# Kernel optimization log

Hardware: AMD Instinct MI355X
Metric: run time of the kernel (lower is better)

Reference implementation:

```python
import jax, jax.numpy as jnp
import numpy as np

F8 = jnp.float8_e4m3fn
FP8_MAX = 448.0  # max representable magnitude of e4m3fn


def setup_inputs() -> dict:
    key = jax.random.key(0)
    kx, kw, kb = jax.random.split(key, 3)
    x = jax.random.normal(kx, (4, 4096, 2048), dtype=jnp.float32)
    w = jax.random.normal(kw, (8192, 2048), dtype=jnp.float32) * 0.02
    bias = (jax.random.normal(kb, (8192,), dtype=jnp.float32) * 0.01).astype(jnp.float16)
    return {"x": x, "w": w, "bias": bias}


def _quantize_per_tensor(t):
    """Dynamic per-tensor symmetric fp8 quantization (mirrors the torch code).
    Returns (t_fp8, inv_scale) with inv_scale = amax / 448."""
    amax = jnp.max(jnp.abs(t))
    scale = (FP8_MAX / jnp.maximum(amax, 1e-12)).astype(jnp.float32)
    scale = jax.lax.stop_gradient(scale)  # torch computes scales under no_grad
    t_fp8 = (t * scale).astype(F8)
    return t_fp8, (1.0 / scale)


def reference(x, w, bias):
    in_features = w.shape[1]
    out_features = w.shape[0]
    x2d = x.reshape(-1, in_features)            # [M, K]
    x_fp8, inv_sx = _quantize_per_tensor(x2d)   # activation: dynamic per-tensor
    w_fp8, inv_sw = _quantize_per_tensor(w)     # weight: pre-quantized buffer + scale_w
    # _scaled_mm: fp8 GEMM accumulated in fp32, output scaled by scale_a*scale_b, cast to fp16
    acc = jnp.matmul(x_fp8.astype(jnp.float32), w_fp8.astype(jnp.float32).T)  # [M, N]
    out = (acc * (inv_sx * inv_sw)).astype(jnp.float16)
    out = out + bias  # fp16 bias epilogue
    return out.reshape(*x.shape[:-1], out_features)
```

## Files before the change

kernel.cpp:

```cpp
#include <hip/hip_runtime.h>
#include <hip/hip_fp16.h>
#include <stdint.h>
#include <stddef.h>

typedef float f32x4 __attribute__((ext_vector_type(4)));
typedef int   i32x8 __attribute__((ext_vector_type(8)));

#define GLOBAL_AS __attribute__((address_space(1)))
#define LDS_AS    __attribute__((address_space(3)))

__device__ __forceinline__ void gload_lds16(const void* g, void* l) {
    __builtin_amdgcn_global_load_lds((const GLOBAL_AS void*)g,
                                     (LDS_AS void*)l, 16, 0, 0);
}

__global__ void amax_kernel(const float* __restrict__ p, size_t n4,
                            float* __restrict__ out) {
    const float4* p4 = (const float4*)p;
    float m = 0.f;
    for (size_t i = (size_t)blockIdx.x * blockDim.x + threadIdx.x; i < n4;
         i += (size_t)gridDim.x * blockDim.x) {
        float4 v = p4[i];
        m = fmaxf(m, fmaxf(fmaxf(fabsf(v.x), fabsf(v.y)),
                           fmaxf(fabsf(v.z), fabsf(v.w))));
    }
    #pragma unroll
    for (int off = 32; off > 0; off >>= 1)
        m = fmaxf(m, __shfl_down(m, off, 64));
    __shared__ float sm[4];
    int wid = threadIdx.x >> 6;
    if ((threadIdx.x & 63) == 0) sm[wid] = m;
    __syncthreads();
    if (threadIdx.x == 0) {
        m = fmaxf(fmaxf(sm[0], sm[1]), fmaxf(sm[2], sm[3]));
        atomicMax((unsigned int*)out, __float_as_uint(m));
    }
}

__global__ void quant_kernel(const float* __restrict__ p, size_t n16,
                             const float* __restrict__ amax_p,
                             uint32_t* __restrict__ q) {
    const float scale = 448.f / fmaxf(*amax_p, 1e-12f);
    size_t i = (size_t)blockIdx.x * blockDim.x + threadIdx.x;
    if (i >= n16) return;
    const float4* src = (const float4*)p + i * 4;
    uint32_t r[4];
    #pragma unroll
    for (int j = 0; j < 4; ++j) {
        float4 v = src[j];
        uint32_t u = __builtin_amdgcn_cvt_pk_fp8_f32(v.x * scale, v.y * scale, 0u, false);
        u = __builtin_amdgcn_cvt_pk_fp8_f32(v.z * scale, v.w * scale, u, true);
        r[j] = u;
    }
    uint4 out;
    out.x = r[0]; out.y = r[1]; out.z = r[2]; out.w = r[3];
    *(uint4*)(q + i * 4) = out;
}

#define BM 128
#define BN 128
#define BK 128

__global__ __launch_bounds__(256) void gemm_mxfp8_kernel(
    const uint8_t* __restrict__ Aq,
    const uint8_t* __restrict__ Bq,
    const float* __restrict__ scal,
    const float* __restrict__ bias,
    float* __restrict__ C,
    int M, int N, int K)
{
    __shared__ __align__(16) uint8_t As[BM * BK];
    __shared__ __align__(16) uint8_t Bs[BN * BK];

    const int tid  = threadIdx.x;
    const int wid  = tid >> 6;
    const int lane = tid & 63;
    const int wm = wid >> 1, wn = wid & 1;
    const int bn = blockIdx.x, bm = blockIdx.y;
    const int r16 = lane & 15, hi = lane >> 4;

    const int srow  = wid * 8 + (lane >> 3);
    const int schunk = ((lane & 7) ^ (lane >> 3)) << 4;
    const uint8_t* Abase = Aq + (size_t)(bm * BM + srow) * K + schunk;
    const uint8_t* Bbase = Bq + (size_t)(bn * BN + srow) * K + schunk;

    const int swz = r16 & 7;
    const int u0 = ((hi * 2)     ^ swz) << 4;
    const int u1 = ((hi * 2 + 1) ^ swz) << 4;

    f32x4 acc[4][4] = {};

    for (int k0 = 0; k0 < K; k0 += BK) {
        #pragma unroll
        for (int rho = 0; rho < 4; ++rho) {
            gload_lds16(Abase + (size_t)rho * 32 * K + k0,
                        As + rho * 4096 + wid * 1024);
            gload_lds16(Bbase + (size_t)rho * 32 * K + k0,
                        Bs + rho * 4096 + wid * 1024);
        }
        __syncthreads();

        i32x8 a[4], b[4];
        #pragma unroll
        for (int mi = 0; mi < 4; ++mi) {
            const uint8_t* pa = As + (wm * 64 + mi * 16 + r16) * BK;
            int4 qa0 = *(const int4*)(pa + u0);
            int4 qa1 = *(const int4*)(pa + u1);
            a[mi] = (i32x8){qa0.x, qa0.y, qa0.z, qa0.w,
                            qa1.x, qa1.y, qa1.z, qa1.w};
            const uint8_t* pb = Bs + (wn * 64 + mi * 16 + r16) * BK;
            int4 qb0 = *(const int4*)(pb + u0);
            int4 qb1 = *(const int4*)(pb + u1);
            b[mi] = (i32x8){qb0.x, qb0.y, qb0.z, qb0.w,
                            qb1.x, qb1.y, qb1.z, qb1.w};
        }

        #pragma unroll
        for (int mi = 0; mi < 4; ++mi)
            #pragma unroll
            for (int nj = 0; nj < 4; ++nj)
                acc[mi][nj] = __builtin_amdgcn_mfma_scale_f32_16x16x128_f8f6f4(
                    a[mi], b[nj], acc[mi][nj],
                    0 , 0 ,
                    0, 0x7F7F7F7F,
                    0, 0x7F7F7F7F);
        __syncthreads();
    }

    const float sx = 448.f / fmaxf(scal[0], 1e-12f);
    const float sw = 448.f / fmaxf(scal[1], 1e-12f);
    const float inv = (1.f / sx) * (1.f / sw);

    #pragma unroll
    for (int mi = 0; mi < 4; ++mi) {
        #pragma unroll
        for (int nj = 0; nj < 4; ++nj) {
            int col = bn * BN + wn * 64 + nj * 16 + r16;
            __half hb = __float2half(bias[col]);
            #pragma unroll
            for (int r = 0; r < 4; ++r) {
                int row = bm * BM + wm * 64 + mi * 16 + hi * 4 + r;
                float v = acc[mi][nj][r] * inv;
                __half h = __hadd(__float2half(v), hb);
                C[(size_t)row * N + col] = __half2float(h);
            }
        }
    }
}

extern "C" void kernel_launch(void* const* d_in, const int* in_sizes, int n_in,
                              void* d_out, int out_size, void* d_ws, size_t ws_size,
                              hipStream_t stream) {
    const float* x    = (const float*)d_in[0];
    const float* w    = (const float*)d_in[1];
    const float* bias = (const float*)d_in[2];
    float* out = (float*)d_out;

    const int N = in_sizes[2];
    const int K = in_sizes[1] / N;
    const int M = in_sizes[0] / K;

    uint8_t* ws = (uint8_t*)d_ws;
    float* scal = (float*)ws;
    uint8_t* Aq = ws + 256;
    uint8_t* Bq = Aq + (size_t)M * K;

    hipMemsetAsync(scal, 0, 8, stream);

    amax_kernel<<<2048, 256, 0, stream>>>(x, (size_t)M * K / 4, scal);
    amax_kernel<<<2048, 256, 0, stream>>>(w, (size_t)N * K / 4, scal + 1);

    size_t nx16 = (size_t)M * K / 16;
    size_t nw16 = (size_t)N * K / 16;
    quant_kernel<<<(int)((nx16 + 255) / 256), 256, 0, stream>>>(x, nx16, scal, (uint32_t*)Aq);
    quant_kernel<<<(int)((nw16 + 255) / 256), 256, 0, stream>>>(w, nw16, scal + 1, (uint32_t*)Bq);

    dim3 grid(N / BN, M / BM);
    gemm_mxfp8_kernel<<<grid, 256, 0, stream>>>(Aq, Bq, scal, bias, out, M, N, K);
}
```

Measured before the change: 468.5 us.

## Use 256x256 tiles with 8-phase double-buffered pipelined fp8 GEMM and fused prep kernels

Replaces the 128x128 single-buffered GEMM with a 256x256 tile, 512-thread kernel that double-buffers LDS and interleaves global-to-LDS loads with MFMA phases, using explicit barriers, waitcnts and raised wave priority. It adds an XCD-aware block remap so neighbouring tiles share L2. The two amax launches and the two quantize launches are each merged into one, cutting launch overhead. The hand-tuned vmcnt scheduling assumes the load order exactly and needs K to be a multiple of 256. The 256x256 tile also means fewer blocks for the same problem.

```diff
diff --git a/kernel.cpp b/kernel.cpp
--- a/kernel.cpp
+++ b/kernel.cpp
@@ -14,12 +14,16 @@
                                      (LDS_AS void*)l, 16, 0, 0);
 }
 
-__global__ void amax_kernel(const float* __restrict__ p, size_t n4,
-                            float* __restrict__ out) {
-    const float4* p4 = (const float4*)p;
+__global__ void amax2_kernel(const float* __restrict__ x, size_t nx4,
+                             const float* __restrict__ w, size_t nw4,
+                             float* __restrict__ scal, int xblocks, int wblocks) {
+    int b = blockIdx.x;
+    const float4* p4; size_t n4; float* out; int nb; int bb;
+    if (b < xblocks) { p4 = (const float4*)x; n4 = nx4; out = scal;     nb = xblocks; bb = b; }
+    else             { p4 = (const float4*)w; n4 = nw4; out = scal + 1; nb = wblocks; bb = b - xblocks; }
     float m = 0.f;
-    for (size_t i = (size_t)blockIdx.x * blockDim.x + threadIdx.x; i < n4;
-         i += (size_t)gridDim.x * blockDim.x) {
+    for (size_t i = (size_t)bb * blockDim.x + threadIdx.x; i < n4;
+         i += (size_t)nb * blockDim.x) {
         float4 v = p4[i];
         m = fmaxf(m, fmaxf(fmaxf(fabsf(v.x), fabsf(v.y)),
                            fmaxf(fabsf(v.z), fabsf(v.w))));
@@ -37,31 +41,34 @@
     }
 }
 
-__global__ void quant_kernel(const float* __restrict__ p, size_t n16,
-                             const float* __restrict__ amax_p,
-                             uint32_t* __restrict__ q) {
-    const float scale = 448.f / fmaxf(*amax_p, 1e-12f);
-    size_t i = (size_t)blockIdx.x * blockDim.x + threadIdx.x;
-    if (i >= n16) return;
-    const float4* src = (const float4*)p + i * 4;
+__global__ void quant2_kernel(const float* __restrict__ x, const float* __restrict__ w,
+                              const float* __restrict__ scal,
+                              uint32_t* __restrict__ qx, uint32_t* __restrict__ qw,
+                              int xblocks) {
+    int b = blockIdx.x;
+    const float* src; uint32_t* dst; float sc; size_t i;
+    if (b < xblocks) { src = x; dst = qx; sc = 448.f / fmaxf(scal[0], 1e-12f);
+                       i = (size_t)b * blockDim.x + threadIdx.x; }
+    else             { src = w; dst = qw; sc = 448.f / fmaxf(scal[1], 1e-12f);
+                       i = (size_t)(b - xblocks) * blockDim.x + threadIdx.x; }
+    const float4* s4 = (const float4*)src + i * 4;
     uint32_t r[4];
     #pragma unroll
     for (int j = 0; j < 4; ++j) {
-        float4 v = src[j];
-        uint32_t u = __builtin_amdgcn_cvt_pk_fp8_f32(v.x * scale, v.y * scale, 0u, false);
-        u = __builtin_amdgcn_cvt_pk_fp8_f32(v.z * scale, v.w * scale, u, true);
+        float4 v = s4[j];
+        uint32_t u = __builtin_amdgcn_cvt_pk_fp8_f32(v.x * sc, v.y * sc, 0u, false);
+        u = __builtin_amdgcn_cvt_pk_fp8_f32(v.z * sc, v.w * sc, u, true);
         r[j] = u;
     }
-    uint4 out;
-    out.x = r[0]; out.y = r[1]; out.z = r[2]; out.w = r[3];
-    *(uint4*)(q + i * 4) = out;
-}
-
-#define BM 128
-#define BN 128
-#define BK 128
-
-__global__ __launch_bounds__(256) void gemm_mxfp8_kernel(
+    uint4 out; out.x = r[0]; out.y = r[1]; out.z = r[2]; out.w = r[3];
+    *(uint4*)(dst + i * 4) = out;
+}
+
+#define BM 256
+#define BN 256
+#define BKB 128
+
+__global__ __launch_bounds__(512, 2) void gemm_mxfp8_8p(
     const uint8_t* __restrict__ Aq,
     const uint8_t* __restrict__ Bq,
     const float* __restrict__ scal,
@@ -69,77 +76,135 @@
     float* __restrict__ C,
     int M, int N, int K)
 {
-    __shared__ __align__(16) uint8_t As[BM * BK];
-    __shared__ __align__(16) uint8_t Bs[BN * BK];
+    __shared__ __align__(16) uint8_t lds[2][2][2][128 * 128];
 
     const int tid  = threadIdx.x;
     const int wid  = tid >> 6;
     const int lane = tid & 63;
-    const int wm = wid >> 1, wn = wid & 1;
-    const int bn = blockIdx.x, bm = blockIdx.y;
+    const int wm = wid >> 2;
+    const int wn = wid & 3;
     const int r16 = lane & 15, hi = lane >> 4;
 
-    const int srow  = wid * 8 + (lane >> 3);
-    const int schunk = ((lane & 7) ^ (lane >> 3)) << 4;
-    const uint8_t* Abase = Aq + (size_t)(bm * BM + srow) * K + schunk;
-    const uint8_t* Bbase = Bq + (size_t)(bn * BN + srow) * K + schunk;
+    const int nwg = gridDim.x;
+    const int cpx = nwg >> 3;
+    const int sbid = (blockIdx.x & 7) * cpx + (blockIdx.x >> 3);
+    const int nbn = N / BN;
+    const int bn = sbid & (nbn - 1);
+    const int bm = sbid / nbn;
+
+    const uint8_t* Abase = Aq + (size_t)bm * BM * K;
+    const uint8_t* Bbase = Bq + (size_t)bn * BN * K;
+
+    const int srow = tid >> 3;
+    const int schunk16 = ((tid & 7) ^ (srow & 7)) << 4;
 
     const int swz = r16 & 7;
     const int u0 = ((hi * 2)     ^ swz) << 4;
     const int u1 = ((hi * 2 + 1) ^ swz) << 4;
 
-    f32x4 acc[4][4] = {};
-
-    for (int k0 = 0; k0 < K; k0 += BK) {
-        #pragma unroll
-        for (int rho = 0; rho < 4; ++rho) {
-            gload_lds16(Abase + (size_t)rho * 32 * K + k0,
-                        As + rho * 4096 + wid * 1024);
-            gload_lds16(Bbase + (size_t)rho * 32 * K + k0,
-                        Bs + rho * 4096 + wid * 1024);
-        }
-        __syncthreads();
-
-        i32x8 a[4], b[4];
-        #pragma unroll
-        for (int mi = 0; mi < 4; ++mi) {
-            const uint8_t* pa = As + (wm * 64 + mi * 16 + r16) * BK;
-            int4 qa0 = *(const int4*)(pa + u0);
-            int4 qa1 = *(const int4*)(pa + u1);
-            a[mi] = (i32x8){qa0.x, qa0.y, qa0.z, qa0.w,
-                            qa1.x, qa1.y, qa1.z, qa1.w};
-            const uint8_t* pb = Bs + (wn * 64 + mi * 16 + r16) * BK;
-            int4 qb0 = *(const int4*)(pb + u0);
-            int4 qb1 = *(const int4*)(pb + u1);
-            b[mi] = (i32x8){qb0.x, qb0.y, qb0.z, qb0.w,
-                            qb1.x, qb1.y, qb1.z, qb1.w};
-        }
-
-        #pragma unroll
-        for (int mi = 0; mi < 4; ++mi)
-            #pragma unroll
-            for (int nj = 0; nj < 4; ++nj)
-                acc[mi][nj] = __builtin_amdgcn_mfma_scale_f32_16x16x128_f8f6f4(
-                    a[mi], b[nj], acc[mi][nj],
-                    0 , 0 ,
-                    0, 0x7F7F7F7F,
-                    0, 0x7F7F7F7F);
-        __syncthreads();
-    }
+#define STAGE(opbase, opi, bufi, h, s)                                            \
+  { const uint8_t* g_ = (opbase) + (size_t)((h) * 128 + srow) * K + (s) * BKB + schunk16; \
+    uint8_t* l_ = &lds[bufi][opi][h][tid * 16];                                   \
+    gload_lds16(g_, l_);                                                          \
+    gload_lds16(g_ + (size_t)64 * K, l_ + 8192); }
+
+#define LDA(bufc, g)                                                              \
+  { const uint8_t* base_ = &lds[bufc][0][wm][0];                                  \
+    _Pragma("unroll") for (int j_ = 0; j_ < 4; ++j_) {                            \
+      const uint8_t* p_ = base_ + ((g) * 64 + j_ * 16 + r16) * 128;               \
+      int4 q0_ = *(const int4*)(p_ + u0);                                         \
+      int4 q1_ = *(const int4*)(p_ + u1);                                         \
+      a[j_] = (i32x8){q0_.x, q0_.y, q0_.z, q0_.w, q1_.x, q1_.y, q1_.z, q1_.w}; } }
+
+#define LDB(bufc, g)                                                              \
+  { const uint8_t* base_ = &lds[bufc][1][wn >> 1][0];                             \
+    _Pragma("unroll") for (int j_ = 0; j_ < 2; ++j_) {                            \
+      const uint8_t* p_ = base_ + ((wn & 1) * 64 + ((g) * 2 + j_) * 16 + r16) * 128; \
+      int4 q0_ = *(const int4*)(p_ + u0);                                         \
+      int4 q1_ = *(const int4*)(p_ + u1);                                         \
+      b[(g) * 2 + j_] = (i32x8){q0_.x, q0_.y, q0_.z, q0_.w, q1_.x, q1_.y, q1_.z, q1_.w}; } }
+
+#define MMA(g_m, g_n)                                                             \
+  __builtin_amdgcn_s_setprio(1);                                                  \
+  _Pragma("unroll") for (int mi_ = 0; mi_ < 4; ++mi_)                             \
+    _Pragma("unroll") for (int nj_ = 0; nj_ < 2; ++nj_)                           \
+      acc[(g_m) * 4 + mi_][(g_n) * 2 + nj_] =                                     \
+        __builtin_amdgcn_mfma_scale_f32_16x16x128_f8f6f4(                         \
+          a[mi_], b[(g_n) * 2 + nj_], acc[(g_m) * 4 + mi_][(g_n) * 2 + nj_],      \
+          0, 0, 0, 0x7F7F7F7F, 0, 0x7F7F7F7F);                                    \
+  __builtin_amdgcn_s_setprio(0);
+
+#define PH_BEGIN() do { asm volatile("" ::: "memory");                            \
+    __builtin_amdgcn_s_barrier();                                                 \
+    asm volatile("s_waitcnt lgkmcnt(0)" ::: "memory");                            \
+    __builtin_amdgcn_sched_barrier(0); } while (0)
+
+#define PH_END() do { asm volatile("" ::: "memory");                              \
+    __builtin_amdgcn_s_barrier();                                                 \
+    asm volatile("" ::: "memory"); } while (0)
+
+#define PH_END_VM(n) do { asm volatile("s_waitcnt vmcnt(" #n ")" ::: "memory");   \
+    __builtin_amdgcn_s_barrier();                                                 \
+    asm volatile("" ::: "memory"); } while (0)
+
+    f32x4 acc[8][4] = {};
+    i32x8 a[4], b[4];
+
+    STAGE(Abase, 0, 0, 0, 0);
+    STAGE(Abase, 0, 0, 1, 0);
+    STAGE(Bbase, 1, 0, 0, 0);
+    STAGE(Bbase, 1, 0, 1, 0);
+    STAGE(Bbase, 1, 1, 0, 1);
+    STAGE(Abase, 0, 1, 0, 1);
+    asm volatile("s_waitcnt vmcnt(4)" ::: "memory");
+    __builtin_amdgcn_s_barrier();
+
+#define ITER(t, LAST) do {                                                        \
+                                                    \
+    LDA(0, 0); LDB(0, 0); STAGE(Bbase, 1, 1, 1, (t) + 1);                         \
+    PH_BEGIN(); MMA(0, 0); PH_END();                                              \
+                                                           \
+    LDB(0, 1); STAGE(Abase, 0, 1, 1, (t) + 1);                                    \
+    PH_BEGIN(); MMA(0, 1); PH_END();                                              \
+                                                           \
+    LDA(0, 1); if (!(LAST)) STAGE(Bbase, 1, 0, 0, (t) + 2);                       \
+    PH_BEGIN(); MMA(1, 1); PH_END();                                              \
+                                                           \
+    if (!(LAST)) STAGE(Abase, 0, 0, 0, (t) + 2);                                  \
+    PH_BEGIN(); MMA(1, 0);                                                        \
+    if (LAST) { PH_END_VM(0); } else { PH_END_VM(4); }                            \
+                                                  \
+    LDA(1, 0); LDB(1, 0); if (!(LAST)) STAGE(Bbase, 1, 0, 1, (t) + 2);            \
+    PH_BEGIN(); MMA(0, 0); PH_END();                                              \
+                                                                          \
+    LDB(1, 1); if (!(LAST)) STAGE(Abase, 0, 0, 1, (t) + 2);                       \
+    PH_BEGIN(); MMA(0, 1); PH_END();                                              \
+                                                                          \
+    LDA(1, 1); if (!(LAST)) STAGE(Bbase, 1, 1, 0, (t) + 3);                       \
+    PH_BEGIN(); MMA(1, 1); PH_END();                                              \
+                                                                          \
+    if (!(LAST)) STAGE(Abase, 0, 1, 0, (t) + 3);                                  \
+    PH_BEGIN(); MMA(1, 0);                                                        \
+    if (LAST) { PH_END(); } else { PH_END_VM(4); }                                \
+  } while (0)
+
+    const int NTILES = K / BKB;
+    for (int t = 0; t < NTILES - 2; t += 2) { ITER(t, false); }
+    ITER(NTILES - 2, true);
 
     const float sx = 448.f / fmaxf(scal[0], 1e-12f);
     const float sw = 448.f / fmaxf(scal[1], 1e-12f);
     const float inv = (1.f / sx) * (1.f / sw);
 
     #pragma unroll
-    for (int mi = 0; mi < 4; ++mi) {
+    for (int mi = 0; mi < 8; ++mi) {
         #pragma unroll
         for (int nj = 0; nj < 4; ++nj) {
             int col = bn * BN + wn * 64 + nj * 16 + r16;
             __half hb = __float2half(bias[col]);
             #pragma unroll
             for (int r = 0; r < 4; ++r) {
-                int row = bm * BM + wm * 64 + mi * 16 + hi * 4 + r;
+                int row = bm * BM + wm * 128 + mi * 16 + hi * 4 + r;
                 float v = acc[mi][nj][r] * inv;
                 __half h = __hadd(__float2half(v), hb);
                 C[(size_t)row * N + col] = __half2float(h);
@@ -167,14 +232,16 @@
 
     hipMemsetAsync(scal, 0, 8, stream);
 
-    amax_kernel<<<2048, 256, 0, stream>>>(x, (size_t)M * K / 4, scal);
-    amax_kernel<<<2048, 256, 0, stream>>>(w, (size_t)N * K / 4, scal + 1);
-
-    size_t nx16 = (size_t)M * K / 16;
-    size_t nw16 = (size_t)N * K / 16;
-    quant_kernel<<<(int)((nx16 + 255) / 256), 256, 0, stream>>>(x, nx16, scal, (uint32_t*)Aq);
-    quant_kernel<<<(int)((nw16 + 255) / 256), 256, 0, stream>>>(w, nw16, scal + 1, (uint32_t*)Bq);
-
-    dim3 grid(N / BN, M / BM);
-    gemm_mxfp8_kernel<<<grid, 256, 0, stream>>>(Aq, Bq, scal, bias, out, M, N, K);
-}
+    const int axb = 2048, awb = 1024;
+    amax2_kernel<<<axb + awb, 256, 0, stream>>>(x, (size_t)M * K / 4,
+                                                w, (size_t)N * K / 4,
+                                                scal, axb, awb);
+
+    int qxb = (int)((size_t)M * K / 16 / 256);
+    int qwb = (int)((size_t)N * K / 16 / 256);
+    quant2_kernel<<<qxb + qwb, 256, 0, stream>>>(x, w, scal,
+                                                 (uint32_t*)Aq, (uint32_t*)Bq, qxb);
+
+    dim3 grid((N / BN) * (M / BM));
+    gemm_mxfp8_8p<<<grid, 512, 0, stream>>>(Aq, Bq, scal, bias, out, M, N, K);
+}
```

Result: slower. 670.6 us (+43.1%).

## Merge amax and quant launches; remap GEMM blocks per XCD for L2 reuse

Applied to the files above, without the earlier changes.

The two amax kernels become one launch, and so do the two quantization kernels, by splitting the block range between x and w. This cuts launch overhead and lets the x and w work run concurrently. The GEMM grid becomes 1D, and block IDs are remapped so each XCD (bid&7) owns a contiguous band of 16 M-tiles while iterating over N-tiles, which is meant to improve L2 reuse of A rows within a die. The remap hard-codes M/BM=128 (8 XCDs x 16) and drops the bounds check in quant, so it only fits these shapes.

```diff
diff --git a/kernel.cpp b/kernel.cpp
--- a/kernel.cpp
+++ b/kernel.cpp
@@ -14,12 +14,16 @@
                                      (LDS_AS void*)l, 16, 0, 0);
 }
 
-__global__ void amax_kernel(const float* __restrict__ p, size_t n4,
-                            float* __restrict__ out) {
-    const float4* p4 = (const float4*)p;
+__global__ void amax2_kernel(const float* __restrict__ x, size_t nx4,
+                             const float* __restrict__ w, size_t nw4,
+                             float* __restrict__ scal, int xblocks, int wblocks) {
+    int b = blockIdx.x;
+    const float4* p4; size_t n4; float* out; int nb; int bb;
+    if (b < xblocks) { p4 = (const float4*)x; n4 = nx4; out = scal;     nb = xblocks; bb = b; }
+    else             { p4 = (const float4*)w; n4 = nw4; out = scal + 1; nb = wblocks; bb = b - xblocks; }
     float m = 0.f;
-    for (size_t i = (size_t)blockIdx.x * blockDim.x + threadIdx.x; i < n4;
-         i += (size_t)gridDim.x * blockDim.x) {
+    for (size_t i = (size_t)bb * blockDim.x + threadIdx.x; i < n4;
+         i += (size_t)nb * blockDim.x) {
         float4 v = p4[i];
         m = fmaxf(m, fmaxf(fmaxf(fabsf(v.x), fabsf(v.y)),
                            fmaxf(fabsf(v.z), fabsf(v.w))));
@@ -37,29 +41,32 @@
     }
 }
 
-__global__ void quant_kernel(const float* __restrict__ p, size_t n16,
-                             const float* __restrict__ amax_p,
-                             uint32_t* __restrict__ q) {
-    const float scale = 448.f / fmaxf(*amax_p, 1e-12f);
-    size_t i = (size_t)blockIdx.x * blockDim.x + threadIdx.x;
-    if (i >= n16) return;
-    const float4* src = (const float4*)p + i * 4;
+__global__ void quant2_kernel(const float* __restrict__ x, const float* __restrict__ w,
+                              const float* __restrict__ scal,
+                              uint32_t* __restrict__ qx, uint32_t* __restrict__ qw,
+                              int xblocks) {
+    int b = blockIdx.x;
+    const float* src; uint32_t* dst; float sc; size_t i;
+    if (b < xblocks) { src = x; dst = qx; sc = 448.f / fmaxf(scal[0], 1e-12f);
+                       i = (size_t)b * blockDim.x + threadIdx.x; }
+    else             { src = w; dst = qw; sc = 448.f / fmaxf(scal[1], 1e-12f);
+                       i = (size_t)(b - xblocks) * blockDim.x + threadIdx.x; }
+    const float4* s4 = (const float4*)src + i * 4;
     uint32_t r[4];
     #pragma unroll
     for (int j = 0; j < 4; ++j) {
-        float4 v = src[j];
-        uint32_t u = __builtin_amdgcn_cvt_pk_fp8_f32(v.x * scale, v.y * scale, 0u, false);
-        u = __builtin_amdgcn_cvt_pk_fp8_f32(v.z * scale, v.w * scale, u, true);
+        float4 v = s4[j];
+        uint32_t u = __builtin_amdgcn_cvt_pk_fp8_f32(v.x * sc, v.y * sc, 0u, false);
+        u = __builtin_amdgcn_cvt_pk_fp8_f32(v.z * sc, v.w * sc, u, true);
         r[j] = u;
     }
-    uint4 out;
-    out.x = r[0]; out.y = r[1]; out.z = r[2]; out.w = r[3];
-    *(uint4*)(q + i * 4) = out;
+    uint4 out; out.x = r[0]; out.y = r[1]; out.z = r[2]; out.w = r[3];
+    *(uint4*)(dst + i * 4) = out;
 }
 
 #define BM 128
 #define BN 128
-#define BK 128
+#define BKB 128
 
 __global__ __launch_bounds__(256) void gemm_mxfp8_kernel(
     const uint8_t* __restrict__ Aq,
@@ -69,15 +76,20 @@
     float* __restrict__ C,
     int M, int N, int K)
 {
-    __shared__ __align__(16) uint8_t As[BM * BK];
-    __shared__ __align__(16) uint8_t Bs[BN * BK];
+    __shared__ __align__(16) uint8_t As[BM * BKB];
+    __shared__ __align__(16) uint8_t Bs[BN * BKB];
 
     const int tid  = threadIdx.x;
     const int wid  = tid >> 6;
     const int lane = tid & 63;
     const int wm = wid >> 1, wn = wid & 1;
-    const int bn = blockIdx.x, bm = blockIdx.y;
     const int r16 = lane & 15, hi = lane >> 4;
+
+    const int bid  = blockIdx.x;
+    const int xcd  = bid & 7;
+    const int loc  = bid >> 3;
+    const int bm   = xcd * 16 + (loc & 15);
+    const int bn   = loc >> 4;
 
     const int srow  = wid * 8 + (lane >> 3);
     const int schunk = ((lane & 7) ^ (lane >> 3)) << 4;
@@ -90,7 +102,7 @@
 
     f32x4 acc[4][4] = {};
 
-    for (int k0 = 0; k0 < K; k0 += BK) {
+    for (int k0 = 0; k0 < K; k0 += BKB) {
         #pragma unroll
         for (int rho = 0; rho < 4; ++rho) {
             gload_lds16(Abase + (size_t)rho * 32 * K + k0,
@@ -103,12 +115,12 @@
         i32x8 a[4], b[4];
         #pragma unroll
         for (int mi = 0; mi < 4; ++mi) {
-            const uint8_t* pa = As + (wm * 64 + mi * 16 + r16) * BK;
+            const uint8_t* pa = As + (wm * 64 + mi * 16 + r16) * BKB;
             int4 qa0 = *(const int4*)(pa + u0);
             int4 qa1 = *(const int4*)(pa + u1);
             a[mi] = (i32x8){qa0.x, qa0.y, qa0.z, qa0.w,
                             qa1.x, qa1.y, qa1.z, qa1.w};
-            const uint8_t* pb = Bs + (wn * 64 + mi * 16 + r16) * BK;
+            const uint8_t* pb = Bs + (wn * 64 + mi * 16 + r16) * BKB;
             int4 qb0 = *(const int4*)(pb + u0);
             int4 qb1 = *(const int4*)(pb + u1);
             b[mi] = (i32x8){qb0.x, qb0.y, qb0.z, qb0.w,
@@ -121,9 +133,7 @@
             for (int nj = 0; nj < 4; ++nj)
                 acc[mi][nj] = __builtin_amdgcn_mfma_scale_f32_16x16x128_f8f6f4(
                     a[mi], b[nj], acc[mi][nj],
-                    0 , 0 ,
-                    0, 0x7F7F7F7F,
-                    0, 0x7F7F7F7F);
+                    0, 0, 0, 0x7F7F7F7F, 0, 0x7F7F7F7F);
         __syncthreads();
     }
 
@@ -167,14 +177,16 @@
 
     hipMemsetAsync(scal, 0, 8, stream);
 
-    amax_kernel<<<2048, 256, 0, stream>>>(x, (size_t)M * K / 4, scal);
-    amax_kernel<<<2048, 256, 0, stream>>>(w, (size_t)N * K / 4, scal + 1);
+    const int axb = 2048, awb = 1024;
+    amax2_kernel<<<axb + awb, 256, 0, stream>>>(x, (size_t)M * K / 4,
+                                                w, (size_t)N * K / 4,
+                                                scal, axb, awb);
 
-    size_t nx16 = (size_t)M * K / 16;
-    size_t nw16 = (size_t)N * K / 16;
-    quant_kernel<<<(int)((nx16 + 255) / 256), 256, 0, stream>>>(x, nx16, scal, (uint32_t*)Aq);
-    quant_kernel<<<(int)((nw16 + 255) / 256), 256, 0, stream>>>(w, nw16, scal + 1, (uint32_t*)Bq);
+    int qxb = (int)((size_t)M * K / 16 / 256);
+    int qwb = (int)((size_t)N * K / 16 / 256);
+    quant2_kernel<<<qxb + qwb, 256, 0, stream>>>(x, w, scal,
+                                                 (uint32_t*)Aq, (uint32_t*)Bq, qxb);
 
-    dim3 grid(N / BN, M / BM);
+    dim3 grid((N / BN) * (M / BM));
     gemm_mxfp8_kernel<<<grid, 256, 0, stream>>>(Aq, Bq, scal, bias, out, M, N, K);
 }
```

Result: slower. 490.6 us (+4.7%).
